# Kernel tuning notes

Hardware: AMD Instinct MI355X
Metric: run time of the kernel (lower is better)

## Reference

```python
import jax, jax.numpy as jnp
import numpy as np

N_WAY = 2
K_SHOT = 5
C = 320
NPTS = 2048
NQ = 2
K_PROTO = 100  # hardcoded k=100 in forward
N_CLS = N_WAY + 1
SIGMA = 1.0
NEG = -1e9


def _l2norm(x, eps=1e-8):
    return x / (jnp.linalg.norm(x, axis=-1, keepdims=True) + eps)


def _class_prototypes(feat, mask, k):
    """Multi-prototype masked pooling for one class.
    feat: [M, C] point features; mask: [M] float (1 = belongs to class).
    Picks k masked seed points, assigns every masked point to its
    nearest (cosine) seed, and returns the k masked cluster means.
    """
    M = feat.shape[0]
    # deterministic seeds: first k masked points (tie-break by index)
    score = mask - jnp.arange(M, dtype=feat.dtype) * 1e-9
    _, seed_idx = jax.lax.top_k(score, k)
    seeds = feat[seed_idx]                      # [k, C]
    sim = _l2norm(feat) @ _l2norm(seeds).T      # [M, k]
    assign = jnp.argmax(sim, axis=1)            # [M]
    onehot = jax.nn.one_hot(assign, k, dtype=feat.dtype) * mask[:, None]  # [M, k]
    num = onehot.T @ feat                       # [k, C]
    den = onehot.sum(axis=0)[:, None] + 1e-8
    return num / den


def _fg_prototypes(support_feat, fg_mask, k):
    # support_feat [n_way, k_shot, C, N] -> per-class point sets [n_way, k_shot*N, C]
    feat = support_feat.transpose(0, 1, 3, 2).reshape(N_WAY, -1, C)
    m = fg_mask.reshape(N_WAY, -1).astype(feat.dtype)
    protos = jax.vmap(lambda f, mm: _class_prototypes(f, mm, k))(feat, m)  # [n_way, k, C]
    labels = jnp.repeat(jnp.arange(1, N_WAY + 1), k)                        # classes 1..n_way
    return protos.reshape(-1, C), jax.nn.one_hot(labels, N_CLS, dtype=feat.dtype)


def _bg_prototypes(support_feat, bg_mask, k):
    feat = support_feat.transpose(0, 1, 3, 2).reshape(-1, C)   # all shots pooled
    m = bg_mask.reshape(-1).astype(feat.dtype)
    protos = _class_prototypes(feat, m, k)                      # [k, C]
    labels = jnp.zeros((k,), dtype=jnp.int32)                   # class 0 = background
    return protos, jax.nn.one_hot(labels, N_CLS, dtype=feat.dtype)


def _predict(prototypes, proto_onehot, qfeat, qlabels):
    # cosine similarity [M, P], per-class max over that class's prototypes
    sim = (_l2norm(qfeat) @ _l2norm(prototypes).T) / SIGMA        # [M, P]
    cls_mask = proto_onehot.T[None] > 0                            # [1, ncls, P]
    pred = jnp.max(jnp.where(cls_mask, sim[:, None, :], NEG), axis=-1)  # [M, ncls]
    logp = jax.nn.log_softmax(pred, axis=-1)
    loss = -jnp.mean(jnp.take_along_axis(logp, qlabels.reshape(-1, 1), axis=1))
    query_pred = pred.reshape(NQ, NPTS, N_CLS).transpose(0, 2, 1)  # [NQ, ncls, NPTS]
    return loss, query_pred


def reference(support_feat, query_feat, support_y, query_y):
    fg_mask = support_y
    bg_mask = 1 - support_y
    fg_protos, fg_labels = _fg_prototypes(support_feat, fg_mask, K_PROTO)
    bg_protos, bg_labels = _bg_prototypes(support_feat, bg_mask, K_PROTO)
    prototypes = jnp.concatenate([bg_protos, fg_protos], axis=0)           # [P, C]
    proto_labels = jnp.concatenate([bg_labels, fg_labels], axis=0)         # [P, ncls]

    qfeat = query_feat.transpose(0, 2, 1).reshape(-1, C)                   # [NQ*NPTS, C]
    loss, query_pred = _predict(prototypes, proto_labels, qfeat, query_y)
    # the forward adds computeCrossEntropyLoss(query_pred, query_y): same CE again
    loss = loss * 2.0

    # post-hoc per-point confidence thresholding (vectorized Python loop)
    qp = jnp.concatenate([query_pred[0], query_pred[1]], axis=-1)          # [ncls, NQ*NPTS]
    predictions = jnp.argmax(qp, axis=0)
    confidences = jnp.max(qp, axis=0)
    final = jnp.where(confidences > jnp.mean(confidences), predictions, -1)
    final_labels = jnp.stack([final[:NPTS], final[NPTS:]], axis=0)         # [2, NPTS]
    return loss, query_pred, final_labels


def setup_inputs() -> dict:
    key = jax.random.key(0)
    k1, k2, k3, k4 = jax.random.split(key, 4)
    return {
        "support_feat": jax.random.normal(k1, (N_WAY, K_SHOT, C, NPTS), dtype=jnp.float32),
        "query_feat": jax.random.normal(k2, (NQ, C, NPTS), dtype=jnp.float32),
        "support_y": jax.random.randint(k3, (N_WAY, K_SHOT, NPTS), 0, 2, dtype=jnp.int32),
        "query_y": jax.random.randint(k4, (NQ, NPTS), 0, 3, dtype=jnp.int32),
    }
```

## Files before the change

### kernel.cpp

```cpp
#include <hip/hip_runtime.h>
#include <math.h>

#define C 320
#define NPTS 2048
#define SUPPTS 20480
#define QPTS 4096
#define KP 100
#define NCLS 3
#define PSTRIDE 300

__global__ __launch_bounds__(64) void k_protoseed(const float* __restrict__ sup,
                                                  const int* __restrict__ sy,
                                                  float* __restrict__ pbufT,
                                                  int* __restrict__ cntG) {
    int p    = blockIdx.x;
    int lane = threadIdx.x;
    if (lane == 0) cntG[p] = 0;
    int prob = (p < 100) ? 2 : ((p < 200) ? 0 : 1);
    int rank = (p < 100) ? p : ((p < 200) ? p - 100 : p - 200);
    int M    = (prob == 2) ? SUPPTS : 10240;
    int base = (prob == 1) ? 10240 : 0;
    int found = 0, sp = 0;
    for (int chunk = 0; chunk < M; chunk += 64) {
        int yy = sy[base + chunk + lane];
        int m  = (prob == 2) ? (1 - yy) : yy;
        unsigned long long bal = __ballot(m != 0);
        int cnt = __popcll(bal);
        if (found + cnt > rank) {
            int need = rank - found;
            int prefix = __popcll(bal & ((1ull << lane) - 1ull));
            unsigned long long match = __ballot(m && (prefix == need));
            int pos = __ffsll((unsigned long long)match) - 1;
            sp = base + chunk + pos;
            break;
        }
        found += cnt;
    }
    const float* fb = sup + ((size_t)(sp >> 11) * C) * NPTS + (sp & 2047);
    float v[5]; float s = 0.f;
    #pragma unroll
    for (int i = 0; i < 5; i++) {
        v[i] = fb[(size_t)(lane + i * 64) * NPTS];
        s += v[i] * v[i];
    }
    #pragma unroll
    for (int off = 32; off > 0; off >>= 1) s += __shfl_down(s, off);
    s = __shfl(s, 0);
    float r = 1.0f / (sqrtf(s) + 1e-8f);
    #pragma unroll
    for (int i = 0; i < 5; i++)
        pbufT[(size_t)(lane + i * 64) * PSTRIDE + p] = v[i] * r;
}

__global__ __launch_bounds__(256) void k_assign(const float* __restrict__ sup,
                                                const int* __restrict__ sy,
                                                const float* __restrict__ pbT,
                                                float* __restrict__ pmaxv,
                                                int* __restrict__ pmaxj) {
    __shared__ float shp[2 * C * 12 + 16];
    int b = blockIdx.x, jt = blockIdx.y, tid = threadIdx.x;
    int w = (b >= 40) ? 1 : 0;
    int colf = 100 + w * 100 + jt * 10;
    int colb = jt * 10;
    const int BGOFF = C * 12 + 16;
    for (int i = tid; i < C * 10; i += 256) {
        int c = i / 10, j = i % 10;
        shp[c * 12 + j]         = pbT[(size_t)c * PSTRIDE + colf + j];
        shp[BGOFF + c * 12 + j] = pbT[(size_t)c * PSTRIDE + colb + j];
    }
    int g = b * 256 + tid;
    int sel = sy[g] ? 0 : BGOFF;
    __syncthreads();
    const float* fb = sup + ((size_t)(g >> 11) * C) * NPTS + (g & 2047);
    float acc[10];
    #pragma unroll
    for (int j = 0; j < 10; j++) acc[j] = 0.f;
    float pf[8];
    #pragma unroll
    for (int k = 0; k < 8; k++) pf[k] = fb[(size_t)k * NPTS];
    for (int cc = 0; cc < C; cc += 8) {
        float cur[8];
        #pragma unroll
        for (int k = 0; k < 8; k++) cur[k] = pf[k];
        if (cc + 8 < C) {
            #pragma unroll
            for (int k = 0; k < 8; k++) pf[k] = fb[(size_t)(cc + 8 + k) * NPTS];
        }
        #pragma unroll
        for (int k = 0; k < 8; k++) {
            const float* row = &shp[sel + (cc + k) * 12];
            float4 p0 = ((const float4*)row)[0];
            float4 p1 = ((const float4*)row)[1];
            float2 p2 = *(const float2*)(row + 8);
            float px = cur[k];
            acc[0] += px * p0.x; acc[1] += px * p0.y;
            acc[2] += px * p0.z; acc[3] += px * p0.w;
            acc[4] += px * p1.x; acc[5] += px * p1.y;
            acc[6] += px * p1.z; acc[7] += px * p1.w;
            acc[8] += px * p2.x; acc[9] += px * p2.y;
        }
    }
    float bv = acc[0]; int bj = 0;
    #pragma unroll
    for (int j = 1; j < 10; j++) {
        if (acc[j] > bv) { bv = acc[j]; bj = j; }
    }
    size_t a0 = (size_t)jt * 20480 + g;
    pmaxv[a0] = bv;
    pmaxj[a0] = jt * 10 + bj;
}

__global__ __launch_bounds__(256) void k_combine_dst(const float* __restrict__ pmaxv,
                                                     const int* __restrict__ pmaxj,
                                                     const int* __restrict__ sy,
                                                     int* __restrict__ dst,
                                                     float* __restrict__ loss,
                                                     int* __restrict__ cntG) {
    int g = blockIdx.x * 256 + threadIdx.x;
    if (g == 0) loss[0] = 0.f;
    if (g == 1) loss[1] = 0.f;
    float bv = pmaxv[g]; int bj = pmaxj[g];
    #pragma unroll
    for (int t = 1; t < 10; t++) {
        float v = pmaxv[(size_t)t * 20480 + g];
        if (v > bv) { bv = v; bj = pmaxj[(size_t)t * 20480 + g]; }
    }
    int way = (g >= 10240) ? 1 : 0;
    int dv = sy[g] ? (100 + way * 100 + bj) : bj;
    dst[g] = dv;
    atomicAdd(&cntG[dv], 1);
}

__global__ __launch_bounds__(256) void k_accum_lds(const float* __restrict__ sup,
                                                   const int* __restrict__ dst,
                                                   float* __restrict__ part) {
    __shared__ float bins[4 * 200 * 16];
    __shared__ int   dl[1024];
    int bx = blockIdx.x;
    int by = blockIdx.y;
    int tid = threadIdx.x;
    int ws = bx >> 1, half = bx & 1;
    int wmask = (ws >= 5) ? 1 : 0;
    int c0 = by * 16;

    int4 d4 = *(const int4*)(dst + ws * 2048 + half * 1024 + 4 * tid);
    dl[4 * tid + 0] = (d4.x < 100) ? d4.x : (d4.x - wmask * 100);
    dl[4 * tid + 1] = (d4.y < 100) ? d4.y : (d4.y - wmask * 100);
    dl[4 * tid + 2] = (d4.z < 100) ? d4.z : (d4.z - wmask * 100);
    dl[4 * tid + 3] = (d4.w < 100) ? d4.w : (d4.w - wmask * 100);
    for (int i = tid; i < 4 * 200 * 16; i += 256) bins[i] = 0.f;
    __syncthreads();

    int wv = tid >> 6, lane = tid & 63;
    int ch = lane & 15, pq = lane >> 4;
    float* mybins = bins + wv * 3200;
    const int* dlp = dl + wv * 256 + pq;
    const float* fb = sup + ((size_t)(ws * C + c0 + ch)) * NPTS + half * 1024 + wv * 256 + pq;

    int   b_cur = dlp[0];
    float f_cur = fb[0];
    for (int it = 0; it < 64; it++) {
        int nidx = (it < 63) ? (it + 1) * 4 : 0;
        int   b_nxt = dlp[nidx];
        float f_nxt = fb[nidx];
        int b0 = __builtin_amdgcn_readlane(b_cur, 0);
        int b1 = __builtin_amdgcn_readlane(b_cur, 16);
        int b2 = __builtin_amdgcn_readlane(b_cur, 32);
        int b3 = __builtin_amdgcn_readlane(b_cur, 48);
        bool dup = (b0 == b1) | (b0 == b2) | (b0 == b3) |
                   (b1 == b2) | (b1 == b3) | (b2 == b3);
        int addr = b_cur * 16 + ch;
        if (!dup) {
            mybins[addr] += f_cur;
        } else {
            unsafeAtomicAdd(&mybins[addr], f_cur);
        }
        b_cur = b_nxt; f_cur = f_nxt;
    }
    __syncthreads();

    for (int i = tid; i < 3200; i += 256) {
        int bin = i >> 4, c = i & 15;
        float s = bins[bin * 16 + c] + bins[3200 + bin * 16 + c]
                + bins[6400 + bin * 16 + c] + bins[9600 + bin * 16 + c];
        int ct8 = by * 2 + (c >> 3);
        part[(size_t)(bx * 40 + ct8) * 1600 + bin * 8 + (c & 7)] = s;
    }
}

__global__ __launch_bounds__(64) void k_reduce_proto(const float* __restrict__ part,
                                                     const int* __restrict__ cntG,
                                                     float* __restrict__ phatT) {
    int d   = blockIdx.x;
    int tid = threadIdx.x;
    int local, s0, ns;
    if (d < 100)      { local = d;       s0 = 0;  ns = 20; }
    else if (d < 200) { local = d;       s0 = 0;  ns = 10; }
    else              { local = d - 100; s0 = 10; ns = 10; }
    float dn = (float)cntG[d];
    float inv = 1.0f / (dn + 1e-8f);
    float vals[5]; float sq = 0.f;
    #pragma unroll
    for (int i = 0; i < 5; i++) {
        int c = tid + i * 64;
        int ct = c >> 3, cl = c & 7;
        float s = 0.f;
        for (int k = 0; k < ns; k++)
            s += part[(size_t)((s0 + k) * 40 + ct) * 1600 + local * 8 + cl];
        float v = s * inv;
        vals[i] = v; sq += v * v;
    }
    #pragma unroll
    for (int off = 32; off > 0; off >>= 1) sq += __shfl_down(sq, off);
    sq = __shfl(sq, 0);
    float rn = 1.0f / (sqrtf(sq) + 1e-8f);
    #pragma unroll
    for (int i = 0; i < 5; i++)
        phatT[(size_t)(tid + i * 64) * PSTRIDE + d] = vals[i] * rn;
}

__global__ __launch_bounds__(256) void k_qpartial(const float* __restrict__ qry,
                                                  const float* __restrict__ phT,
                                                  float* __restrict__ qmaxv,
                                                  float* __restrict__ qrn) {
    __shared__ float shp[C * 16];
    __shared__ float red[3 * 64 * 45];
    int pb = blockIdx.x, jt = blockIdx.y, tid = threadIdx.x;
    int wave = tid >> 6, lane = tid & 63;
    int j0 = jt * 10;
    for (int i = tid; i < C * 10; i += 256) {
        int j = i % 10, c = i / 10;
        shp[c * 16 + j] = phT[(size_t)c * PSTRIDE + j0 + j];
    }
    __syncthreads();
    int m = pb * 256 + lane * 4;
    int c0 = wave * 80;
    const float* fb = qry + ((size_t)(m >> 11) * C + c0) * NPTS + (m & 2047);
    float acc[4][10];
    #pragma unroll
    for (int p = 0; p < 4; p++)
        #pragma unroll
        for (int j = 0; j < 10; j++) acc[p][j] = 0.f;
    float qn[4] = {0.f, 0.f, 0.f, 0.f};
    float4 pf[8];
    #pragma unroll
    for (int k = 0; k < 8; k++) pf[k] = *(const float4*)(fb + (size_t)k * NPTS);
    for (int cc = 0; cc < 80; cc += 8) {
        float4 cur[8];
        #pragma unroll
        for (int k = 0; k < 8; k++) cur[k] = pf[k];
        if (cc + 8 < 80) {
            #pragma unroll
            for (int k = 0; k < 8; k++) pf[k] = *(const float4*)(fb + (size_t)(cc + 8 + k) * NPTS);
        }
        #pragma unroll
        for (int k = 0; k < 8; k++) {
            const float* row = &shp[(c0 + cc + k) * 16];
            float4 p0 = ((const float4*)row)[0];
            float4 p1 = ((const float4*)row)[1];
            float2 p2 = ((const float2*)row)[4];
            float pr[10] = {p0.x,p0.y,p0.z,p0.w,p1.x,p1.y,p1.z,p1.w,p2.x,p2.y};
            float4 cv = cur[k];
            if (jt == 0) {
                qn[0] += cv.x*cv.x; qn[1] += cv.y*cv.y; qn[2] += cv.z*cv.z; qn[3] += cv.w*cv.w;
            }
            #pragma unroll
            for (int j = 0; j < 10; j++) {
                acc[0][j] += cv.x * pr[j];
                acc[1][j] += cv.y * pr[j];
                acc[2][j] += cv.z * pr[j];
                acc[3][j] += cv.w * pr[j];
            }
        }
    }
    if (wave > 0) {
        float* my = red + ((wave - 1) * 64 + lane) * 45;
        #pragma unroll
        for (int p = 0; p < 4; p++)
            #pragma unroll
            for (int j = 0; j < 10; j++) my[p * 10 + j] = acc[p][j];
        #pragma unroll
        for (int p = 0; p < 4; p++) my[40 + p] = qn[p];
    }
    __syncthreads();
    if (wave == 0) {
        #pragma unroll
        for (int w = 0; w < 3; w++) {
            const float* my = red + (w * 64 + lane) * 45;
            #pragma unroll
            for (int p = 0; p < 4; p++)
                #pragma unroll
                for (int j = 0; j < 10; j++) acc[p][j] += my[p * 10 + j];
            #pragma unroll
            for (int p = 0; p < 4; p++) qn[p] += my[40 + p];
        }
        #pragma unroll
        for (int p = 0; p < 4; p++) {
            float bv = acc[p][0];
            #pragma unroll
            for (int j = 1; j < 10; j++) bv = fmaxf(bv, acc[p][j]);
            qmaxv[(size_t)(m + p) * 30 + jt] = bv;
        }
        if (jt == 0) {
            #pragma unroll
            for (int p = 0; p < 4; p++) qrn[m + p] = 1.0f / (sqrtf(qn[p]) + 1e-8f);
        }
    }
}

__global__ __launch_bounds__(256) void k_pred(const float* __restrict__ qmaxv,
                                              const float* __restrict__ qrn,
                                              const int* __restrict__ qy,
                                              float* __restrict__ out,
                                              float* __restrict__ lossacc,
                                              float* __restrict__ cbuf,
                                              int* __restrict__ lbuf) {
    __shared__ float redL[256];
    __shared__ float redC[256];
    int tid = threadIdx.x;
    int m = blockIdx.x * 256 + tid;
    float rn = qrn[m];
    float pred[NCLS];
    #pragma unroll
    for (int cls = 0; cls < NCLS; cls++) {
        float g = qmaxv[(size_t)m * 30 + cls * 10];
        #pragma unroll
        for (int t = 1; t < 10; t++) g = fmaxf(g, qmaxv[(size_t)m * 30 + cls * 10 + t]);
        pred[cls] = rn * g;
    }
    int q = m >> 11, n = m & 2047;
    #pragma unroll
    for (int cls = 0; cls < NCLS; cls++)
        out[1 + ((size_t)(q * NCLS + cls)) * NPTS + n] = pred[cls];
    float mx = fmaxf(pred[0], fmaxf(pred[1], pred[2]));
    float lse = mx + logf(expf(pred[0] - mx) + expf(pred[1] - mx) + expf(pred[2] - mx));
    int lab = 0; float cf = pred[0];
    if (pred[1] > cf) { cf = pred[1]; lab = 1; }
    if (pred[2] > cf) { cf = pred[2]; lab = 2; }
    cbuf[m] = cf; lbuf[m] = lab;
    redL[tid] = lse - pred[qy[m]];
    redC[tid] = cf;
    __syncthreads();
    for (int off = 128; off > 0; off >>= 1) {
        if (tid < off) { redL[tid] += redL[tid + off]; redC[tid] += redC[tid + off]; }
        __syncthreads();
    }
    if (tid == 0) {
        atomicAdd(&lossacc[0], redL[0]);
        atomicAdd(&lossacc[1], redC[0]);
    }
}

__global__ __launch_bounds__(256) void k_final(const float* __restrict__ cbuf,
                                               const int* __restrict__ lbuf,
                                               const float* __restrict__ lossacc,
                                               float* __restrict__ out) {
    int m = blockIdx.x * 256 + threadIdx.x;
    float mean = lossacc[1] / (float)QPTS;
    float cf = cbuf[m];
    out[1 + 2 * NCLS * NPTS + m] = (cf > mean) ? (float)lbuf[m] : -1.0f;
    if (m == 0) out[0] = 2.0f * lossacc[0] / (float)QPTS;
}

extern "C" void kernel_launch(void* const* d_in, const int* in_sizes, int n_in,
                              void* d_out, int out_size, void* d_ws, size_t ws_size,
                              hipStream_t stream) {
    const float* sup = (const float*)d_in[0];
    const float* qry = (const float*)d_in[1];
    const int*   sy  = (const int*)d_in[2];
    const int*   qy  = (const int*)d_in[3];
    float* out = (float*)d_out;

    float* f      = (float*)d_ws;
    float* qrn    = f;
    float* cnt    = qrn + QPTS;
    int*   cntG   = (int*)cnt;
    float* pbufT  = cnt + 4000;
    float* phatT  = pbufT + 96000;
    float* loss   = phatT + 96000;
    int*   dstb   = (int*)(loss + 4);
    float* trans  = (float*)(dstb + SUPPTS);
    float* pmaxv  = trans;
    int*   pmaxj  = (int*)(pmaxv + 204800);
    float* part   = trans;
    float* qmaxv  = trans;
    float* cbuf   = qmaxv + 122880;
    int*   lbuf   = (int*)(cbuf + QPTS);

    k_protoseed<<<300, 64, 0, stream>>>(sup, sy, pbufT, cntG);
    {
        dim3 grid(80, 10);
        k_assign<<<grid, 256, 0, stream>>>(sup, sy, pbufT, pmaxv, pmaxj);
    }
    k_combine_dst<<<80, 256, 0, stream>>>(pmaxv, pmaxj, sy, dstb, loss, cntG);
    {
        dim3 grid(20, 20);
        k_accum_lds<<<grid, 256, 0, stream>>>(sup, dstb, part);
    }
    k_reduce_proto<<<300, 64, 0, stream>>>(part, cntG, phatT);
    {
        dim3 grid(16, 30);
        k_qpartial<<<grid, 256, 0, stream>>>(qry, phatT, qmaxv, qrn);
    }
    k_pred<<<16, 256, 0, stream>>>(qmaxv, qrn, qy, out, loss, cbuf, lbuf);
    k_final<<<16, 256, 0, stream>>>(cbuf, lbuf, loss, out);
}
```

Before: 203.2 us.

## Read prototype tiles from global with uniform loads, computing both bg and fg scores

```diff
diff --git a/kernel.cpp b/kernel.cpp
--- a/kernel.cpp
+++ b/kernel.cpp
@@ -11,7 +11,7 @@
 
 __global__ __launch_bounds__(64) void k_protoseed(const float* __restrict__ sup,
                                                   const int* __restrict__ sy,
-                                                  float* __restrict__ pbufT,
+                                                  float* __restrict__ pbP,
                                                   int* __restrict__ cntG) {
     int p    = blockIdx.x;
     int lane = threadIdx.x;
@@ -47,34 +47,28 @@
     for (int off = 32; off > 0; off >>= 1) s += __shfl_down(s, off);
     s = __shfl(s, 0);
     float r = 1.0f / (sqrtf(s) + 1e-8f);
+    int tile, slot;
+    if (p < 100)      { tile = p / 10;              slot = p % 10; }
+    else if (p < 200) { tile = 10 + (p - 100) / 10; slot = (p - 100) % 10; }
+    else              { tile = 20 + (p - 200) / 10; slot = (p - 200) % 10; }
     #pragma unroll
     for (int i = 0; i < 5; i++)
-        pbufT[(size_t)(lane + i * 64) * PSTRIDE + p] = v[i] * r;
+        pbP[(size_t)(lane + i * 64) * 480 + tile * 16 + slot] = v[i] * r;
 }
 
 __global__ __launch_bounds__(256) void k_assign(const float* __restrict__ sup,
-                                                const int* __restrict__ sy,
-                                                const float* __restrict__ pbT,
+                                                const float* __restrict__ pbP,
                                                 float* __restrict__ pmaxv,
                                                 int* __restrict__ pmaxj) {
-    __shared__ float shp[2 * C * 12 + 16];
     int b = blockIdx.x, jt = blockIdx.y, tid = threadIdx.x;
     int w = (b >= 40) ? 1 : 0;
-    int colf = 100 + w * 100 + jt * 10;
-    int colb = jt * 10;
-    const int BGOFF = C * 12 + 16;
-    for (int i = tid; i < C * 10; i += 256) {
-        int c = i / 10, j = i % 10;
-        shp[c * 12 + j]         = pbT[(size_t)c * PSTRIDE + colf + j];
-        shp[BGOFF + c * 12 + j] = pbT[(size_t)c * PSTRIDE + colb + j];
-    }
     int g = b * 256 + tid;
-    int sel = sy[g] ? 0 : BGOFF;
-    __syncthreads();
     const float* fb = sup + ((size_t)(g >> 11) * C) * NPTS + (g & 2047);
-    float acc[10];
-    #pragma unroll
-    for (int j = 0; j < 10; j++) acc[j] = 0.f;
+    const float* rbb = pbP + (size_t)jt * 16;
+    const float* rfb = pbP + (size_t)(10 + w * 10 + jt) * 16;
+    float accB[10], accF[10];
+    #pragma unroll
+    for (int j = 0; j < 10; j++) { accB[j] = 0.f; accF[j] = 0.f; }
     float pf[8];
     #pragma unroll
     for (int k = 0; k < 8; k++) pf[k] = fb[(size_t)k * NPTS];
@@ -88,26 +82,26 @@
         }
         #pragma unroll
         for (int k = 0; k < 8; k++) {
-            const float* row = &shp[sel + (cc + k) * 12];
-            float4 p0 = ((const float4*)row)[0];
-            float4 p1 = ((const float4*)row)[1];
-            float2 p2 = *(const float2*)(row + 8);
+            const float* rb = rbb + (size_t)(cc + k) * 480;
+            const float* rf = rfb + (size_t)(cc + k) * 480;
             float px = cur[k];
-            acc[0] += px * p0.x; acc[1] += px * p0.y;
-            acc[2] += px * p0.z; acc[3] += px * p0.w;
-            acc[4] += px * p1.x; acc[5] += px * p1.y;
-            acc[6] += px * p1.z; acc[7] += px * p1.w;
-            acc[8] += px * p2.x; acc[9] += px * p2.y;
-        }
-    }
-    float bv = acc[0]; int bj = 0;
+            #pragma unroll
+            for (int j = 0; j < 10; j++) {
+                accB[j] += px * rb[j];
+                accF[j] += px * rf[j];
+            }
+        }
+    }
+    float bvB = accB[0]; int bjB = 0;
+    float bvF = accF[0]; int bjF = 0;
     #pragma unroll
     for (int j = 1; j < 10; j++) {
-        if (acc[j] > bv) { bv = acc[j]; bj = j; }
-    }
-    size_t a0 = (size_t)jt * 20480 + g;
-    pmaxv[a0] = bv;
-    pmaxj[a0] = jt * 10 + bj;
+        if (accB[j] > bvB) { bvB = accB[j]; bjB = j; }
+        if (accF[j] > bvF) { bvF = accF[j]; bjF = j; }
+    }
+    size_t a0 = (size_t)jt * 40960 + g;
+    pmaxv[a0] = bvB;          pmaxj[a0] = jt * 10 + bjB;
+    pmaxv[a0 + 20480] = bvF;  pmaxj[a0 + 20480] = jt * 10 + bjF;
 }
 
 __global__ __launch_bounds__(256) void k_combine_dst(const float* __restrict__ pmaxv,
@@ -119,14 +113,18 @@
     int g = blockIdx.x * 256 + threadIdx.x;
     if (g == 0) loss[0] = 0.f;
     if (g == 1) loss[1] = 0.f;
-    float bv = pmaxv[g]; int bj = pmaxj[g];
+    float bvB = pmaxv[g];         int bjB = pmaxj[g];
+    float bvF = pmaxv[20480 + g]; int bjF = pmaxj[20480 + g];
     #pragma unroll
     for (int t = 1; t < 10; t++) {
-        float v = pmaxv[(size_t)t * 20480 + g];
-        if (v > bv) { bv = v; bj = pmaxj[(size_t)t * 20480 + g]; }
+        size_t base = (size_t)t * 40960;
+        float vB = pmaxv[base + g];
+        if (vB > bvB) { bvB = vB; bjB = pmaxj[base + g]; }
+        float vF = pmaxv[base + 20480 + g];
+        if (vF > bvF) { bvF = vF; bjF = pmaxj[base + 20480 + g]; }
     }
     int way = (g >= 10240) ? 1 : 0;
-    int dv = sy[g] ? (100 + way * 100 + bj) : bj;
+    int dv = sy[g] ? (100 + way * 100 + bjF) : bjB;
     dst[g] = dv;
     atomicAdd(&cntG[dv], 1);
 }
@@ -381,16 +379,17 @@
     int*   dstb   = (int*)(loss + 4);
     float* trans  = (float*)(dstb + SUPPTS);
     float* pmaxv  = trans;
-    int*   pmaxj  = (int*)(pmaxv + 204800);
+    int*   pmaxj  = (int*)(pmaxv + 409600);
+    float* pbP    = (float*)(pmaxj + 409600);
     float* part   = trans;
     float* qmaxv  = trans;
     float* cbuf   = qmaxv + 122880;
     int*   lbuf   = (int*)(cbuf + QPTS);
 
-    k_protoseed<<<300, 64, 0, stream>>>(sup, sy, pbufT, cntG);
+    k_protoseed<<<300, 64, 0, stream>>>(sup, sy, pbP, cntG);
     {
         dim3 grid(80, 10);
-        k_assign<<<grid, 256, 0, stream>>>(sup, sy, pbufT, pmaxv, pmaxj);
+        k_assign<<<grid, 256, 0, stream>>>(sup, pbP, pmaxv, pmaxj);
     }
     k_combine_dst<<<80, 256, 0, stream>>>(pmaxv, pmaxj, sy, dstb, loss, cntG);
     {
```

Result: slower. 246.7 us (+21.4%).
